# Performance work log

Measured on AMD Instinct MI355X. Metric: run time of the kernel, lower is better.

The kernel has to match this reference:

```python
import jax, jax.numpy as jnp
import numpy as np

NODE_CARDS = [119, 5, 12, 12, 10, 6, 6, 2, 2]
EDGE_CARDS = [5, 6, 2]
HIDDEN = 256
LAYERS = 5
N = 60000
E = 180000
G = 2048  # num graphs (fixed num_segments)
BN_EPS = 1e-5

_NODE_OFFS = np.concatenate([[0], np.cumsum(NODE_CARDS[:-1])]).astype(np.int32)
_EDGE_OFFS = np.concatenate([[0], np.cumsum(EDGE_CARDS[:-1])]).astype(np.int32)
_NODE_MAX = np.asarray(NODE_CARDS, np.int32) - 1
_EDGE_MAX = np.asarray(EDGE_CARDS, np.int32) - 1


def _cat_sum(x, table, maxs, offs):
    # x: [N, F] int; table: [sum(cards), H] -> [N, H]
    idx = jnp.clip(x, 0, maxs[None, :]) + offs[None, :]
    return table[idx].sum(axis=1)


def setup_inputs() -> dict:
    key = jax.random.key(0)
    ks = jax.random.split(key, 32)
    w = 0.0625  # ~ xavier for 256

    def nrm(k, shape, s=w):
        return jax.random.normal(k, shape, dtype=jnp.float32) * s

    inp = {
        'x': jax.random.randint(ks[0], (N, len(NODE_CARDS)), 0, 119, dtype=jnp.int32),
        'edge_index': jax.random.randint(ks[1], (2, E), 0, N, dtype=jnp.int32),
        'edge_attr': jax.random.randint(ks[2], (E, len(EDGE_CARDS)), 0, 6, dtype=jnp.int32),
        'batch': jnp.sort(jax.random.randint(ks[3], (N,), 0, G, dtype=jnp.int32)),
        # embeddings
        'node_emb': nrm(ks[4], (int(sum(NODE_CARDS)), HIDDEN), 0.1),
        'edge_emb': nrm(ks[5], (int(sum(EDGE_CARDS)), HIDDEN), 0.1),
        'vn_emb': nrm(ks[6], (1, HIDDEN), 0.1),
        # GINE conv: eps + 2-layer MLP per layer (stacked)
        'eps': jnp.zeros((LAYERS,), jnp.float32),
        'W1': nrm(ks[7], (LAYERS, HIDDEN, HIDDEN)),
        'b1': jnp.zeros((LAYERS, HIDDEN), jnp.float32),
        'W2': nrm(ks[8], (LAYERS, HIDDEN, HIDDEN)),
        'b2': jnp.zeros((LAYERS, HIDDEN), jnp.float32),
        # BatchNorm (eval mode: running stats)
        'bn_gamma': jnp.ones((LAYERS, HIDDEN), jnp.float32),
        'bn_beta': jnp.zeros((LAYERS, HIDDEN), jnp.float32),
        'bn_mean': nrm(ks[9], (LAYERS, HIDDEN), 0.02),
        'bn_var': jnp.ones((LAYERS, HIDDEN), jnp.float32),
        # virtual-node MLP per layer
        'vW1': nrm(ks[10], (LAYERS, HIDDEN, HIDDEN)),
        'vb1': jnp.zeros((LAYERS, HIDDEN), jnp.float32),
        'vW2': nrm(ks[11], (LAYERS, HIDDEN, HIDDEN)),
        'vb2': jnp.zeros((LAYERS, HIDDEN), jnp.float32),
        # head MLP (2 layers: hidden->hidden->1)
        'hW1': nrm(ks[12], (HIDDEN, HIDDEN)),
        'hb1': jnp.zeros((HIDDEN,), jnp.float32),
        'hW2': nrm(ks[13], (HIDDEN, 1)),
        'hb2': jnp.zeros((1,), jnp.float32),
    }
    return inp


def reference(x, edge_index, edge_attr, batch,
              node_emb, edge_emb, vn_emb, eps,
              W1, b1, W2, b2,
              bn_gamma, bn_beta, bn_mean, bn_var,
              vW1, vb1, vW2, vb2,
              hW1, hb1, hW2, hb2):
    node_maxs = jnp.asarray(_NODE_MAX)
    node_offs = jnp.asarray(_NODE_OFFS)
    edge_maxs = jnp.asarray(_EDGE_MAX)
    edge_offs = jnp.asarray(_EDGE_OFFS)

    h = _cat_sum(x, node_emb, node_maxs, node_offs)          # [N, H]
    ea = _cat_sum(edge_attr, edge_emb, edge_maxs, edge_offs)  # [E, H]
    src, dst = edge_index[0], edge_index[1]

    vn = jnp.broadcast_to(vn_emb[0], (G, HIDDEN))  # [G, H]

    def mean_pool(h_):
        s = jax.ops.segment_sum(h_, batch, num_segments=G)
        cnt = jax.ops.segment_sum(jnp.ones((h_.shape[0], 1), h_.dtype), batch, num_segments=G)
        return s / jnp.maximum(cnt, 1.0)

    for l in range(LAYERS):
        h = h + vn[batch]
        # GINEConv: msg = relu(x_src + edge_attr); agg scatter-add onto dst
        msg = jax.nn.relu(h[src] + ea)                        # [E, H]
        agg = jax.ops.segment_sum(msg, dst, num_segments=N)   # [N, H]
        z = (1.0 + eps[l]) * h + agg
        z = jax.nn.relu(z @ W1[l] + b1[l]) @ W2[l] + b2[l]
        # BatchNorm1d (eval, running stats)
        z = (z - bn_mean[l]) * (bn_gamma[l] / jnp.sqrt(bn_var[l] + BN_EPS)) + bn_beta[l]
        h = jax.nn.relu(z)
        # virtual-node update
        g = mean_pool(h)
        vn = vn + (jax.nn.relu(g @ vW1[l] + vb1[l]) @ vW2[l] + vb2[l])

    g = mean_pool(h)                                          # [G, H]
    logits = (jax.nn.relu(g @ hW1 + hb1) @ hW2 + hb2).reshape(-1)  # [G]
    return logits
```

## Files before the change

kernel.cpp:

```cpp
#include <hip/hip_runtime.h>

#define NN 60000
#define NE 180000
#define NG 2048
#define NL 5
#define CAP 32

typedef unsigned short u16;
typedef unsigned int u32;
typedef __bf16 bf16x8 __attribute__((ext_vector_type(8)));
typedef float f32x4 __attribute__((ext_vector_type(4)));

__device__ __forceinline__ u16 f2bf(float f) {
    u32 u = __builtin_bit_cast(u32, f);
    u += 0x7FFFu + ((u >> 16) & 1u);
    return (u16)(u >> 16);
}
__device__ __forceinline__ float bf2f(u16 s) {
    return __builtin_bit_cast(float, (u32)s << 16);
}
__device__ __forceinline__ void gload_lds16(const void* g, void* l) {
    __builtin_amdgcn_global_load_lds(
        (const __attribute__((address_space(1))) unsigned int*)g,
        (__attribute__((address_space(3))) unsigned int*)l, 16, 0, 0);
}
__device__ __forceinline__ int swz(int row, int col) {
    return (row << 9) + ((((col >> 3) ^ (row & 7))) << 4) + ((col & 7) << 1);
}

__constant__ int NODE_OFF[9]  = {0, 119, 124, 136, 148, 158, 164, 170, 172};
__constant__ int NODE_MAXC[9] = {118, 4, 11, 11, 9, 5, 5, 1, 1};

__global__ __launch_bounds__(256) void k_prep_weights(
    const float* __restrict__ W1, const float* __restrict__ W2,
    const float* __restrict__ vW1, const float* __restrict__ vW2,
    const float* __restrict__ hW1, u16* __restrict__ Wt)
{
    int mat = blockIdx.x >> 8;
    int n = blockIdx.x & 255;
    int k = threadIdx.x;
    const float* src;
    if (mat < 5)       src = W1 + (size_t)mat * 65536;
    else if (mat < 10) src = W2 + (size_t)(mat - 5) * 65536;
    else if (mat < 15) src = vW1 + (size_t)(mat - 10) * 65536;
    else if (mat < 20) src = vW2 + (size_t)(mat - 15) * 65536;
    else               src = hW1;
    Wt[(size_t)mat * 65536 + n * 256 + k] = f2bf(src[k * 256 + n]);
}

__global__ __launch_bounds__(256) void k_misc(
    const float* __restrict__ eemb, const int* __restrict__ batch,
    const float* __restrict__ vn_emb,
    u16* __restrict__ comb, int* __restrict__ starts,
    float* __restrict__ vn, u16* __restrict__ vnbf, float* __restrict__ gsum)
{
    int b = blockIdx.x;
    if (b < 2048) {
        int i = b * 256 + threadIdx.x;
        float v = vn_emb[i & 255];
        vn[i] = v;
        vnbf[i] = f2bf(v);
        gsum[i] = 0.f;
    } else if (b < 2108) {
        int r = b - 2048, c = threadIdx.x;
        int a0 = r / 12, a1 = (r % 12) / 2, a2 = r & 1;
        comb[r * 256 + c] = f2bf(eemb[a0 * 256 + c] + eemb[(5 + a1) * 256 + c] +
                                 eemb[(11 + a2) * 256 + c]);
    } else {
        int g = (b - 2108) * 256 + threadIdx.x;
        if (g > NG) return;
        int lo = 0, hi = NN;
        while (lo < hi) {
            int mid = (lo + hi) >> 1;
            if (batch[mid] < g) lo = mid + 1; else hi = mid;
        }
        starts[g] = lo;
    }
}

__global__ __launch_bounds__(256) void k_embed(const int* __restrict__ x,
                                               const float* __restrict__ node_emb,
                                               u16* __restrict__ hbf,
                                               int* __restrict__ deg)
{
    int i = blockIdx.x * 4 + (threadIdx.x >> 6);
    if (i >= NN) return;
    if ((threadIdx.x & 63) == 0) deg[i] = 0;
    int c = (threadIdx.x & 63) * 4;
    float4 s = make_float4(0.f, 0.f, 0.f, 0.f);
#pragma unroll
    for (int f = 0; f < 9; ++f) {
        int xv = x[i * 9 + f];
        xv = xv < 0 ? 0 : (xv > NODE_MAXC[f] ? NODE_MAXC[f] : xv);
        const float4 t = *(const float4*)&node_emb[(size_t)(NODE_OFF[f] + xv) * 256 + c];
        s.x += t.x; s.y += t.y; s.z += t.z; s.w += t.w;
    }
    ushort4 o;
    o.x = f2bf(s.x); o.y = f2bf(s.y); o.z = f2bf(s.z); o.w = f2bf(s.w);
    *(ushort4*)&hbf[(size_t)i * 256 + c] = o;
}

__global__ __launch_bounds__(256) void k_bucket(
    const int* __restrict__ src, const int* __restrict__ dst,
    const int* __restrict__ eattr, int* __restrict__ deg, u32* __restrict__ slots)
{
    int e = blockIdx.x * 256 + threadIdx.x;
    if (e >= NE) return;
    int a0 = eattr[e * 3 + 0]; a0 = a0 < 0 ? 0 : (a0 > 4 ? 4 : a0);
    int a1 = eattr[e * 3 + 1]; a1 = a1 < 0 ? 0 : (a1 > 5 ? 5 : a1);
    int a2 = eattr[e * 3 + 2]; a2 = a2 < 0 ? 0 : (a2 > 1 ? 1 : a2);
    u32 code = (u32)(a0 * 12 + a1 * 2 + a2);
    int d = dst[e];
    int p = atomicAdd(&deg[d], 1);
    if (p < CAP) slots[(size_t)d * CAP + p] = (u32)src[e] | (code << 17);
}

__global__ __launch_bounds__(256) void k_agg(
    const u16* __restrict__ hbf, const u16* __restrict__ vnbf,
    const int* __restrict__ batch, const u32* __restrict__ slots,
    const int* __restrict__ deg, const u16* __restrict__ comb,
    u16* __restrict__ Abf, const float* __restrict__ epsp)
{
    int d = blockIdx.x * 4 + (threadIdx.x >> 6);
    int lane = threadIdx.x & 63;
    int c = lane * 4;
    int nd = deg[d];
    nd = nd > CAP ? CAP : nd;

    const u32* sl = slots + (size_t)d * CAP;
    u32 sv_l = (lane < nd) ? sl[lane] : 0u;
    int b_l = (lane < nd) ? batch[sv_l & 0x1FFFFu] : 0;

    float4 acc = make_float4(0.f, 0.f, 0.f, 0.f);
    for (int p = 0; p < nd; ++p) {
        u32 sv = (u32)__shfl((int)sv_l, p);
        int b  = __shfl(b_l, p);
        int s  = (int)(sv & 0x1FFFFu);
        int code = (int)(sv >> 17);
        const ushort4 hv = *(const ushort4*)&hbf[(size_t)s * 256 + c];
        const ushort4 vv = *(const ushort4*)&vnbf[(size_t)b * 256 + c];
        const ushort4 tv = *(const ushort4*)&comb[(size_t)code * 256 + c];
        acc.x += fmaxf(bf2f(hv.x) + bf2f(vv.x) + bf2f(tv.x), 0.f);
        acc.y += fmaxf(bf2f(hv.y) + bf2f(vv.y) + bf2f(tv.y), 0.f);
        acc.z += fmaxf(bf2f(hv.z) + bf2f(vv.z) + bf2f(tv.z), 0.f);
        acc.w += fmaxf(bf2f(hv.w) + bf2f(vv.w) + bf2f(tv.w), 0.f);
    }

    int bd = batch[d];
    float ep = 1.0f + *epsp;
    const ushort4 hd = *(const ushort4*)&hbf[(size_t)d * 256 + c];
    const ushort4 vd = *(const ushort4*)&vnbf[(size_t)bd * 256 + c];
    ushort4 o;
    o.x = f2bf((bf2f(hd.x) + bf2f(vd.x)) * ep + acc.x);
    o.y = f2bf((bf2f(hd.y) + bf2f(vd.y)) * ep + acc.y);
    o.z = f2bf((bf2f(hd.z) + bf2f(vd.z)) * ep + acc.z);
    o.w = f2bf((bf2f(hd.w) + bf2f(vd.w)) * ep + acc.w);
    *(ushort4*)&Abf[(size_t)d * 256 + c] = o;
}

__device__ __forceinline__ void stageW(const u16* __restrict__ W, u16* Bl,
                                       int k0, int tid, int wid)
{
#pragma unroll
    for (int i = 0; i < 4; ++i) {
        int slot = i * 512 + tid;
        int row = slot >> 3, cch = slot & 7;
        int g = cch ^ (row & 7);
        gload_lds16((const char*)W + (size_t)row * 512 + (size_t)k0 * 2 + (g << 4),
                    (char*)Bl + ((i * 512 + wid * 64) << 4));
    }
}

__device__ __forceinline__ void gemm64(const u16* Tl, u16* Bl, const u16* __restrict__ W,
                                       f32x4 (&acc)[2][4], int wm, int wn,
                                       int lane, int tid, int wid)
{
    const int cl = lane & 15;
    for (int k0 = 0; k0 < 256; k0 += 64) {
        __syncthreads();
        stageW(W, Bl, k0, tid, wid);
        __syncthreads();
#pragma unroll
        for (int kw = 0; kw < 2; ++kw) {
            int q = kw * 4 + (lane >> 4);
            int qt = (k0 >> 3) + q;
            bf16x8 af[2], bfr[4];
#pragma unroll
            for (int t = 0; t < 2; ++t) {
                int ar = wm + t * 16 + cl;
                af[t] = __builtin_bit_cast(bf16x8,
                    *(const uint4*)((const char*)Tl + (ar << 9) + ((qt ^ (ar & 7)) << 4)));
            }
#pragma unroll
            for (int t = 0; t < 4; ++t) {
                int br = wn + t * 16 + cl;
                bfr[t] = __builtin_bit_cast(bf16x8,
                    *(const uint4*)((const char*)Bl + (br << 7) + ((q ^ (br & 7)) << 4)));
            }
#pragma unroll
            for (int i = 0; i < 2; ++i)
#pragma unroll
                for (int j = 0; j < 4; ++j)
                    acc[i][j] = __builtin_amdgcn_mfma_f32_16x16x32_bf16(af[i], bfr[j], acc[i][j], 0, 0, 0);
        }
    }
}

__device__ __forceinline__ void writeT(u16* Tl, const f32x4 (&acc)[2][4],
                                       const float* __restrict__ b1,
                                       int wm, int wn, int lane)
{
    const int cl = lane & 15, rg = lane >> 4;
#pragma unroll
    for (int j = 0; j < 4; ++j) {
        int col = wn + j * 16 + cl;
        float bv = b1[col];
#pragma unroll
        for (int i = 0; i < 2; ++i)
#pragma unroll
            for (int r = 0; r < 4; ++r) {
                int row = wm + i * 16 + rg * 4 + r;
                float v = fmaxf(acc[i][j][r] + bv, 0.f);
                *(u16*)((char*)Tl + swz(row, col)) = f2bf(v);
            }
    }
}

__global__ __launch_bounds__(512) void k_mlpP(
    const u16* __restrict__ Abf, u16* __restrict__ hnxt,
    const int* __restrict__ batch,
    const u16* __restrict__ W1t, const u16* __restrict__ W2t,
    const float* __restrict__ b1, const float* __restrict__ b2,
    const float* __restrict__ bng, const float* __restrict__ bnb,
    const float* __restrict__ bnm, const float* __restrict__ bnv,
    float* __restrict__ gsum)
{
    __shared__ __align__(16) u16 Bl[256 * 64];
    __shared__ __align__(16) u16 Tl[64 * 256];
    __shared__ int batchLds[64];
    const int m0 = blockIdx.x * 64;
    const int tid = threadIdx.x, lane = tid & 63, wid = tid >> 6;
    const int wm = (wid >> 2) * 32, wn = (wid & 3) * 64;
    const int cl = lane & 15, rg = lane >> 4;

    if (tid < 64) batchLds[tid] = (m0 + tid < NN) ? batch[m0 + tid] : -1;

#pragma unroll
    for (int i = 0; i < 4; ++i) {
        int slot = i * 512 + tid;
        int row = slot >> 5, cch = slot & 31;
        int g = cch ^ (row & 7);
        gload_lds16((const char*)Abf + (size_t)(m0 + row) * 512 + (g << 4),
                    (char*)Tl + ((i * 512 + wid * 64) << 4));
    }

    f32x4 acc1[2][4] = {};
    gemm64(Tl, Bl, W1t, acc1, wm, wn, lane, tid, wid);
    __syncthreads();
    writeT(Tl, acc1, b1, wm, wn, lane);

    f32x4 acc2[2][4] = {};
    gemm64(Tl, Bl, W2t, acc2, wm, wn, lane, tid, wid);
    __syncthreads();

#pragma unroll
    for (int j = 0; j < 4; ++j) {
        int gn = wn + j * 16 + cl;
        float bv = b2[gn];
        float sc = bng[gn] * rsqrtf(bnv[gn] + 1e-5f);
        float sh = bnb[gn] - bnm[gn] * sc;
#pragma unroll
        for (int i = 0; i < 2; ++i) {
#pragma unroll
            for (int r = 0; r < 4; ++r) {
                int lr = wm + i * 16 + rg * 4 + r;
                int gm = m0 + lr;
                if (gm >= NN) continue;
                float v = acc2[i][j][r] + bv;
                u16 hb = f2bf(fmaxf(v * sc + sh, 0.f));
                hnxt[(size_t)gm * 256 + gn] = hb;
                *(u16*)((char*)Tl + swz(lr, gn)) = hb;
            }
        }
    }
    __syncthreads();

    {
        int col = tid & 255, half = tid >> 8;
        float s = 0.f;
        int gcur = -1;
        int r0 = half * 32;
        for (int r = r0; r < r0 + 32; ++r) {
            int g = batchLds[r];
            if (g < 0) break;
            if (g != gcur) {
                if (gcur >= 0) atomicAdd(&gsum[(size_t)gcur * 256 + col], s);
                gcur = g; s = 0.f;
            }
            s += bf2f(*(const u16*)((const char*)Tl + swz(r, col)));
        }
        if (gcur >= 0) atomicAdd(&gsum[(size_t)gcur * 256 + col], s);
    }
}

__global__ __launch_bounds__(512) void k_vnmlp(
    float* __restrict__ gsum, const int* __restrict__ starts,
    const u16* __restrict__ W1t, const u16* __restrict__ W2t,
    const float* __restrict__ b1, const float* __restrict__ b2,
    float* __restrict__ vn, u16* __restrict__ vnbf)
{
    __shared__ __align__(16) u16 Bl[256 * 64];
    __shared__ __align__(16) u16 Tl[64 * 256];
    const int m0 = blockIdx.x * 64;
    const int tid = threadIdx.x, lane = tid & 63, wid = tid >> 6;
    const int wm = (wid >> 2) * 32, wn = (wid & 3) * 64;
    const int cl = lane & 15, rg = lane >> 4;

    {
        const int c = lane * 4;
#pragma unroll
        for (int n = 0; n < 8; ++n) {
            int row = wid * 8 + n;
            int g = m0 + row;
            float4 sv = *(const float4*)&gsum[(size_t)g * 256 + c];
            *(float4*)&gsum[(size_t)g * 256 + c] = make_float4(0.f, 0.f, 0.f, 0.f);
            float cnt = (float)(starts[g + 1] - starts[g]);
            float inv = 1.0f / fmaxf(cnt, 1.0f);
            ushort4 o;
            o.x = f2bf(sv.x * inv); o.y = f2bf(sv.y * inv);
            o.z = f2bf(sv.z * inv); o.w = f2bf(sv.w * inv);
            *(ushort4*)((char*)Tl + swz(row, c)) = o;
        }
    }
    __syncthreads();

    f32x4 acc1[2][4] = {};
    gemm64(Tl, Bl, W1t, acc1, wm, wn, lane, tid, wid);
    __syncthreads();
    writeT(Tl, acc1, b1, wm, wn, lane);

    f32x4 acc2[2][4] = {};
    gemm64(Tl, Bl, W2t, acc2, wm, wn, lane, tid, wid);

#pragma unroll
    for (int j = 0; j < 4; ++j) {
        int gn = wn + j * 16 + cl;
        float bv = b2[gn];
#pragma unroll
        for (int i = 0; i < 2; ++i) {
#pragma unroll
            for (int r = 0; r < 4; ++r) {
                int gm = m0 + wm + i * 16 + rg * 4 + r;
                size_t idx = (size_t)gm * 256 + gn;
                float nv = vn[idx] + acc2[i][j][r] + bv;
                vn[idx] = nv;
                vnbf[idx] = f2bf(nv);
            }
        }
    }
}

__global__ __launch_bounds__(512) void k_headf(
    const float* __restrict__ gsum, const int* __restrict__ starts,
    const u16* __restrict__ W1t, const float* __restrict__ b1,
    const float* __restrict__ hW2, const float* __restrict__ hb2,
    float* __restrict__ out)
{
    __shared__ __align__(16) u16 Bl[256 * 64];
    __shared__ __align__(16) u16 Tl[64 * 256];
    const int m0 = blockIdx.x * 64;
    const int tid = threadIdx.x, lane = tid & 63, wid = tid >> 6;
    const int wm = (wid >> 2) * 32, wn = (wid & 3) * 64;

    {
        const int c = lane * 4;
#pragma unroll
        for (int n = 0; n < 8; ++n) {
            int row = wid * 8 + n;
            int g = m0 + row;
            float4 sv = *(const float4*)&gsum[(size_t)g * 256 + c];
            float cnt = (float)(starts[g + 1] - starts[g]);
            float inv = 1.0f / fmaxf(cnt, 1.0f);
            ushort4 o;
            o.x = f2bf(sv.x * inv); o.y = f2bf(sv.y * inv);
            o.z = f2bf(sv.z * inv); o.w = f2bf(sv.w * inv);
            *(ushort4*)((char*)Tl + swz(row, c)) = o;
        }
    }
    __syncthreads();

    f32x4 acc1[2][4] = {};
    gemm64(Tl, Bl, W1t, acc1, wm, wn, lane, tid, wid);
    __syncthreads();
    writeT(Tl, acc1, b1, wm, wn, lane);
    __syncthreads();

    int row = tid >> 3, oct = tid & 7;
    float s = 0.f;
#pragma unroll
    for (int c = 0; c < 32; ++c) {
        int col = oct * 32 + c;
        s += bf2f(*(const u16*)((const char*)Tl + swz(row, col))) * hW2[col];
    }
    s += __shfl_down(s, 4);
    s += __shfl_down(s, 2);
    s += __shfl_down(s, 1);
    if (oct == 0) out[m0 + row] = s + hb2[0];
}

extern "C" void kernel_launch(void* const* d_in, const int* in_sizes, int n_in,
                              void* d_out, int out_size, void* d_ws, size_t ws_size,
                              hipStream_t stream)
{
    const int*   x        = (const int*)d_in[0];
    const int*   ei       = (const int*)d_in[1];
    const int*   eattr    = (const int*)d_in[2];
    const int*   batch    = (const int*)d_in[3];
    const float* node_emb = (const float*)d_in[4];
    const float* edge_emb = (const float*)d_in[5];
    const float* vn_emb   = (const float*)d_in[6];
    const float* eps      = (const float*)d_in[7];
    const float* W1       = (const float*)d_in[8];
    const float* b1       = (const float*)d_in[9];
    const float* W2       = (const float*)d_in[10];
    const float* b2       = (const float*)d_in[11];
    const float* bng      = (const float*)d_in[12];
    const float* bnb      = (const float*)d_in[13];
    const float* bnm      = (const float*)d_in[14];
    const float* bnv      = (const float*)d_in[15];
    const float* vW1      = (const float*)d_in[16];
    const float* vb1      = (const float*)d_in[17];
    const float* vW2      = (const float*)d_in[18];
    const float* vb2      = (const float*)d_in[19];
    const float* hW1      = (const float*)d_in[20];
    const float* hb1      = (const float*)d_in[21];
    const float* hW2      = (const float*)d_in[22];
    const float* hb2      = (const float*)d_in[23];
    float* out = (float*)d_out;

    char* ws = (char*)d_ws;
    size_t off = 0;
    auto alloc = [&](size_t b) {
        char* p = ws + off;
        off = (off + b + 255) & ~(size_t)255;
        return p;
    };
    u16*   hbf0 = (u16*)alloc((size_t)NN * 256 * 2);
    u16*   hbf1 = (u16*)alloc((size_t)NN * 256 * 2);
    u16*   Abf  = (u16*)alloc((size_t)NN * 256 * 2);
    float* vn   = (float*)alloc((size_t)NG * 256 * 4);
    u16*   vnbf = (u16*)alloc((size_t)NG * 256 * 2);
    float* gsum = (float*)alloc((size_t)NG * 256 * 4);
    u16*   Wt   = (u16*)alloc((size_t)21 * 65536 * 2);
    int*   starts = (int*)alloc((size_t)(NG + 1) * 4);
    u16*   comb = (u16*)alloc((size_t)60 * 256 * 2);
    int*   deg  = (int*)alloc((size_t)NN * 4);
    u32*   slots = (u32*)alloc((size_t)NN * CAP * 4);

    const int* srcI = ei;
    const int* dstI = ei + NE;

    k_prep_weights<<<21 * 256, 256, 0, stream>>>(W1, W2, vW1, vW2, hW1, Wt);
    k_misc<<<2117, 256, 0, stream>>>(edge_emb, batch, vn_emb, comb, starts, vn, vnbf, gsum);
    k_embed<<<NN / 4, 256, 0, stream>>>(x, node_emb, hbf0, deg);
    k_bucket<<<(NE + 255) / 256, 256, 0, stream>>>(srcI, dstI, eattr, deg, slots);

    const int GBIG = (NN + 63) / 64;
    const int GSM  = NG / 64;

    u16* hcur = hbf0;
    u16* hnxt = hbf1;
    for (int l = 0; l < NL; ++l) {
        k_agg<<<NN / 4, 256, 0, stream>>>(hcur, vnbf, batch, slots, deg, comb, Abf, eps + l);
        k_mlpP<<<GBIG, 512, 0, stream>>>(Abf, hnxt, batch,
                                         Wt + (size_t)(0 + l) * 65536,
                                         Wt + (size_t)(5 + l) * 65536,
                                         b1 + l * 256, b2 + l * 256,
                                         bng + l * 256, bnb + l * 256,
                                         bnm + l * 256, bnv + l * 256,
                                         gsum);
        if (l < NL - 1) {
            k_vnmlp<<<GSM, 512, 0, stream>>>(gsum, starts,
                                             Wt + (size_t)(10 + l) * 65536,
                                             Wt + (size_t)(15 + l) * 65536,
                                             vb1 + l * 256, vb2 + l * 256,
                                             vn, vnbf);
        }
        u16* t = hcur; hcur = hnxt; hnxt = t;
    }
    k_headf<<<GSM, 512, 0, stream>>>(gsum, starts, Wt + (size_t)20 * 65536,
                                     hb1, hW2, hb2, out);
}
```

Baseline: 549.2 us.

## Hold MLP weights in registers with 128-row tiles; widen aggregation to 8 bf16 per lane

The fused MLP kernel now processes 128 rows per block. Each wave keeps its 32-column slices of both weight matrices in registers instead of staging weight tiles through LDS every k-step, and the mean-pool partial sums are taken straight from accumulators. This removes repeated weight staging and its barriers, at the cost of heavy register pressure and fewer blocks. The aggregation kernel also handles two nodes per wave with 16-byte loads per lane, which halves the number of load instructions per edge.

```diff
diff --git a/kernel.cpp b/kernel.cpp
--- a/kernel.cpp
+++ b/kernel.cpp
@@ -18,6 +18,15 @@
 }
 __device__ __forceinline__ float bf2f(u16 s) {
     return __builtin_bit_cast(float, (u32)s << 16);
+}
+__device__ __forceinline__ float bflo(u32 w) {
+    return __builtin_bit_cast(float, w << 16);
+}
+__device__ __forceinline__ float bfhi(u32 w) {
+    return __builtin_bit_cast(float, w & 0xFFFF0000u);
+}
+__device__ __forceinline__ u32 pack2bf(float lo, float hi) {
+    return (u32)f2bf(lo) | ((u32)f2bf(hi) << 16);
 }
 __device__ __forceinline__ void gload_lds16(const void* g, void* l) {
     __builtin_amdgcn_global_load_lds(
@@ -121,112 +130,55 @@
     const int* __restrict__ deg, const u16* __restrict__ comb,
     u16* __restrict__ Abf, const float* __restrict__ epsp)
 {
-    int d = blockIdx.x * 4 + (threadIdx.x >> 6);
-    int lane = threadIdx.x & 63;
-    int c = lane * 4;
+    const int wid = threadIdx.x >> 6, lane = threadIdx.x & 63;
+    const int half = lane >> 5, l32 = lane & 31;
+    const int d = blockIdx.x * 8 + wid * 2 + half;
+    const int c = l32 * 8;
     int nd = deg[d];
     nd = nd > CAP ? CAP : nd;
 
     const u32* sl = slots + (size_t)d * CAP;
-    u32 sv_l = (lane < nd) ? sl[lane] : 0u;
-    int b_l = (lane < nd) ? batch[sv_l & 0x1FFFFu] : 0;
-
-    float4 acc = make_float4(0.f, 0.f, 0.f, 0.f);
+    u32 sv_l = (l32 < nd) ? sl[l32] : 0u;
+    int b_l = (l32 < nd) ? batch[sv_l & 0x1FFFFu] : 0;
+
+    float acc[8] = {0.f, 0.f, 0.f, 0.f, 0.f, 0.f, 0.f, 0.f};
     for (int p = 0; p < nd; ++p) {
-        u32 sv = (u32)__shfl((int)sv_l, p);
-        int b  = __shfl(b_l, p);
+        int srcl = (lane & 32) | p;
+        u32 sv = (u32)__shfl((int)sv_l, srcl);
+        int b  = __shfl(b_l, srcl);
         int s  = (int)(sv & 0x1FFFFu);
         int code = (int)(sv >> 17);
-        const ushort4 hv = *(const ushort4*)&hbf[(size_t)s * 256 + c];
-        const ushort4 vv = *(const ushort4*)&vnbf[(size_t)b * 256 + c];
-        const ushort4 tv = *(const ushort4*)&comb[(size_t)code * 256 + c];
-        acc.x += fmaxf(bf2f(hv.x) + bf2f(vv.x) + bf2f(tv.x), 0.f);
-        acc.y += fmaxf(bf2f(hv.y) + bf2f(vv.y) + bf2f(tv.y), 0.f);
-        acc.z += fmaxf(bf2f(hv.z) + bf2f(vv.z) + bf2f(tv.z), 0.f);
-        acc.w += fmaxf(bf2f(hv.w) + bf2f(vv.w) + bf2f(tv.w), 0.f);
+        const uint4 hv = *(const uint4*)&hbf[(size_t)s * 256 + c];
+        const uint4 vv = *(const uint4*)&vnbf[(size_t)b * 256 + c];
+        const uint4 tv = *(const uint4*)&comb[(size_t)code * 256 + c];
+        const u32* hw = (const u32*)&hv;
+        const u32* vw = (const u32*)&vv;
+        const u32* tw = (const u32*)&tv;
+#pragma unroll
+        for (int e = 0; e < 4; ++e) {
+            acc[e * 2 + 0] += fmaxf(bflo(hw[e]) + bflo(vw[e]) + bflo(tw[e]), 0.f);
+            acc[e * 2 + 1] += fmaxf(bfhi(hw[e]) + bfhi(vw[e]) + bfhi(tw[e]), 0.f);
+        }
     }
 
     int bd = batch[d];
     float ep = 1.0f + *epsp;
-    const ushort4 hd = *(const ushort4*)&hbf[(size_t)d * 256 + c];
-    const ushort4 vd = *(const ushort4*)&vnbf[(size_t)bd * 256 + c];
-    ushort4 o;
-    o.x = f2bf((bf2f(hd.x) + bf2f(vd.x)) * ep + acc.x);
-    o.y = f2bf((bf2f(hd.y) + bf2f(vd.y)) * ep + acc.y);
-    o.z = f2bf((bf2f(hd.z) + bf2f(vd.z)) * ep + acc.z);
-    o.w = f2bf((bf2f(hd.w) + bf2f(vd.w)) * ep + acc.w);
-    *(ushort4*)&Abf[(size_t)d * 256 + c] = o;
-}
-
-__device__ __forceinline__ void stageW(const u16* __restrict__ W, u16* Bl,
-                                       int k0, int tid, int wid)
-{
-#pragma unroll
-    for (int i = 0; i < 4; ++i) {
-        int slot = i * 512 + tid;
-        int row = slot >> 3, cch = slot & 7;
-        int g = cch ^ (row & 7);
-        gload_lds16((const char*)W + (size_t)row * 512 + (size_t)k0 * 2 + (g << 4),
-                    (char*)Bl + ((i * 512 + wid * 64) << 4));
-    }
-}
-
-__device__ __forceinline__ void gemm64(const u16* Tl, u16* Bl, const u16* __restrict__ W,
-                                       f32x4 (&acc)[2][4], int wm, int wn,
-                                       int lane, int tid, int wid)
-{
-    const int cl = lane & 15;
-    for (int k0 = 0; k0 < 256; k0 += 64) {
-        __syncthreads();
-        stageW(W, Bl, k0, tid, wid);
-        __syncthreads();
-#pragma unroll
-        for (int kw = 0; kw < 2; ++kw) {
-            int q = kw * 4 + (lane >> 4);
-            int qt = (k0 >> 3) + q;
-            bf16x8 af[2], bfr[4];
-#pragma unroll
-            for (int t = 0; t < 2; ++t) {
-                int ar = wm + t * 16 + cl;
-                af[t] = __builtin_bit_cast(bf16x8,
-                    *(const uint4*)((const char*)Tl + (ar << 9) + ((qt ^ (ar & 7)) << 4)));
-            }
-#pragma unroll
-            for (int t = 0; t < 4; ++t) {
-                int br = wn + t * 16 + cl;
-                bfr[t] = __builtin_bit_cast(bf16x8,
-                    *(const uint4*)((const char*)Bl + (br << 7) + ((q ^ (br & 7)) << 4)));
-            }
-#pragma unroll
-            for (int i = 0; i < 2; ++i)
-#pragma unroll
-                for (int j = 0; j < 4; ++j)
-                    acc[i][j] = __builtin_amdgcn_mfma_f32_16x16x32_bf16(af[i], bfr[j], acc[i][j], 0, 0, 0);
-        }
-    }
-}
-
-__device__ __forceinline__ void writeT(u16* Tl, const f32x4 (&acc)[2][4],
-                                       const float* __restrict__ b1,
-                                       int wm, int wn, int lane)
-{
-    const int cl = lane & 15, rg = lane >> 4;
-#pragma unroll
-    for (int j = 0; j < 4; ++j) {
-        int col = wn + j * 16 + cl;
-        float bv = b1[col];
-#pragma unroll
-        for (int i = 0; i < 2; ++i)
-#pragma unroll
-            for (int r = 0; r < 4; ++r) {
-                int row = wm + i * 16 + rg * 4 + r;
-                float v = fmaxf(acc[i][j][r] + bv, 0.f);
-                *(u16*)((char*)Tl + swz(row, col)) = f2bf(v);
-            }
-    }
-}
-
-__global__ __launch_bounds__(512) void k_mlpP(
+    const uint4 hd = *(const uint4*)&hbf[(size_t)d * 256 + c];
+    const uint4 vd = *(const uint4*)&vnbf[(size_t)bd * 256 + c];
+    const u32* hw = (const u32*)&hd;
+    const u32* vw = (const u32*)&vd;
+    uint4 o;
+    u32* op = (u32*)&o;
+#pragma unroll
+    for (int e = 0; e < 4; ++e) {
+        float lo = (bflo(hw[e]) + bflo(vw[e])) * ep + acc[e * 2 + 0];
+        float hi = (bfhi(hw[e]) + bfhi(vw[e])) * ep + acc[e * 2 + 1];
+        op[e] = pack2bf(lo, hi);
+    }
+    *(uint4*)&Abf[(size_t)d * 256 + c] = o;
+}
+
+__global__ __launch_bounds__(512, 2) void k_mlp2(
     const u16* __restrict__ Abf, u16* __restrict__ hnxt,
     const int* __restrict__ batch,
     const u16* __restrict__ W1t, const u16* __restrict__ W2t,
@@ -235,71 +187,180 @@
     const float* __restrict__ bnm, const float* __restrict__ bnv,
     float* __restrict__ gsum)
 {
-    __shared__ __align__(16) u16 Bl[256 * 64];
-    __shared__ __align__(16) u16 Tl[64 * 256];
-    __shared__ int batchLds[64];
-    const int m0 = blockIdx.x * 64;
+    __shared__ __align__(16) u16 Tl[128 * 256];
+    __shared__ int batchLds[128];
+    const int m0 = blockIdx.x * 128;
     const int tid = threadIdx.x, lane = tid & 63, wid = tid >> 6;
-    const int wm = (wid >> 2) * 32, wn = (wid & 3) * 64;
+    const int wn = wid * 32;
     const int cl = lane & 15, rg = lane >> 4;
 
-    if (tid < 64) batchLds[tid] = (m0 + tid < NN) ? batch[m0 + tid] : -1;
-
-#pragma unroll
-    for (int i = 0; i < 4; ++i) {
+    if (tid < 128) batchLds[tid] = (m0 + tid < NN) ? batch[m0 + tid] : -1;
+
+    bf16x8 B1[2][8], B2[2][8];
+#pragma unroll
+    for (int j = 0; j < 2; ++j) {
+        const char* w1p = (const char*)W1t + (size_t)(wn + j * 16 + cl) * 512 + (rg << 4);
+        const char* w2p = (const char*)W2t + (size_t)(wn + j * 16 + cl) * 512 + (rg << 4);
+#pragma unroll
+        for (int ks = 0; ks < 8; ++ks) {
+            B1[j][ks] = __builtin_bit_cast(bf16x8, *(const uint4*)(w1p + ks * 64));
+            B2[j][ks] = __builtin_bit_cast(bf16x8, *(const uint4*)(w2p + ks * 64));
+        }
+    }
+
+#pragma unroll
+    for (int i = 0; i < 8; ++i) {
         int slot = i * 512 + tid;
         int row = slot >> 5, cch = slot & 31;
         int g = cch ^ (row & 7);
         gload_lds16((const char*)Abf + (size_t)(m0 + row) * 512 + (g << 4),
                     (char*)Tl + ((i * 512 + wid * 64) << 4));
     }
-
-    f32x4 acc1[2][4] = {};
-    gemm64(Tl, Bl, W1t, acc1, wm, wn, lane, tid, wid);
-    __syncthreads();
-    writeT(Tl, acc1, b1, wm, wn, lane);
-
-    f32x4 acc2[2][4] = {};
-    gemm64(Tl, Bl, W2t, acc2, wm, wn, lane, tid, wid);
-    __syncthreads();
-
-#pragma unroll
-    for (int j = 0; j < 4; ++j) {
+    __syncthreads();
+
+    f32x4 acc[8][2] = {};
+#pragma unroll
+    for (int ks = 0; ks < 8; ++ks) {
+#pragma unroll
+        for (int i = 0; i < 8; ++i) {
+            int ar = i * 16 + cl;
+            int ch = ks * 4 + rg;
+            bf16x8 af = __builtin_bit_cast(bf16x8,
+                *(const uint4*)((const char*)Tl + (ar << 9) + ((ch ^ (ar & 7)) << 4)));
+#pragma unroll
+            for (int j = 0; j < 2; ++j)
+                acc[i][j] = __builtin_amdgcn_mfma_f32_16x16x32_bf16(af, B1[j][ks], acc[i][j], 0, 0, 0);
+        }
+    }
+    __syncthreads();
+
+#pragma unroll
+    for (int j = 0; j < 2; ++j) {
+        int col = wn + j * 16 + cl;
+        float bv = b1[col];
+#pragma unroll
+        for (int i = 0; i < 8; ++i)
+#pragma unroll
+            for (int r = 0; r < 4; ++r) {
+                int row = i * 16 + rg * 4 + r;
+                float v = fmaxf(acc[i][j][r] + bv, 0.f);
+                *(u16*)((char*)Tl + swz(row, col)) = f2bf(v);
+            }
+    }
+    __syncthreads();
+
+#pragma unroll
+    for (int i = 0; i < 8; ++i)
+#pragma unroll
+        for (int j = 0; j < 2; ++j)
+            acc[i][j] = f32x4{0.f, 0.f, 0.f, 0.f};
+#pragma unroll
+    for (int ks = 0; ks < 8; ++ks) {
+#pragma unroll
+        for (int i = 0; i < 8; ++i) {
+            int ar = i * 16 + cl;
+            int ch = ks * 4 + rg;
+            bf16x8 af = __builtin_bit_cast(bf16x8,
+                *(const uint4*)((const char*)Tl + (ar << 9) + ((ch ^ (ar & 7)) << 4)));
+#pragma unroll
+            for (int j = 0; j < 2; ++j)
+                acc[i][j] = __builtin_amdgcn_mfma_f32_16x16x32_bf16(af, B2[j][ks], acc[i][j], 0, 0, 0);
+        }
+    }
+
+#pragma unroll
+    for (int j = 0; j < 2; ++j) {
         int gn = wn + j * 16 + cl;
         float bv = b2[gn];
         float sc = bng[gn] * rsqrtf(bnv[gn] + 1e-5f);
         float sh = bnb[gn] - bnm[gn] * sc;
-#pragma unroll
-        for (int i = 0; i < 2; ++i) {
-#pragma unroll
-            for (int r = 0; r < 4; ++r) {
-                int lr = wm + i * 16 + rg * 4 + r;
-                int gm = m0 + lr;
-                if (gm >= NN) continue;
-                float v = acc2[i][j][r] + bv;
-                u16 hb = f2bf(fmaxf(v * sc + sh, 0.f));
-                hnxt[(size_t)gm * 256 + gn] = hb;
-                *(u16*)((char*)Tl + swz(lr, gn)) = hb;
-            }
-        }
-    }
-    __syncthreads();
-
-    {
-        int col = tid & 255, half = tid >> 8;
         float s = 0.f;
         int gcur = -1;
-        int r0 = half * 32;
-        for (int r = r0; r < r0 + 32; ++r) {
-            int g = batchLds[r];
-            if (g < 0) break;
-            if (g != gcur) {
-                if (gcur >= 0) atomicAdd(&gsum[(size_t)gcur * 256 + col], s);
-                gcur = g; s = 0.f;
+#pragma unroll
+        for (int i = 0; i < 8; ++i) {
+#pragma unroll
+            for (int r = 0; r < 4; ++r) {
+                int row = i * 16 + rg * 4 + r;
+                int g = batchLds[row];
+                float v = acc[i][j][r] + bv;
+                u16 hb = f2bf(fmaxf(v * sc + sh, 0.f));
+                if (g >= 0) hnxt[(size_t)(m0 + row) * 256 + gn] = hb;
+                if (g != gcur) {
+                    if (gcur >= 0) atomicAdd(&gsum[(size_t)gcur * 256 + gn], s);
+                    gcur = g; s = 0.f;
+                }
+                if (g >= 0) s += bf2f(hb);
             }
-            s += bf2f(*(const u16*)((const char*)Tl + swz(r, col)));
-        }
-        if (gcur >= 0) atomicAdd(&gsum[(size_t)gcur * 256 + col], s);
+        }
+        if (gcur >= 0) atomicAdd(&gsum[(size_t)gcur * 256 + gn], s);
+    }
+}
+
+__device__ __forceinline__ void stageW(const u16* __restrict__ W, u16* Bl,
+                                       int k0, int tid, int wid)
+{
+#pragma unroll
+    for (int i = 0; i < 4; ++i) {
+        int slot = i * 512 + tid;
+        int row = slot >> 3, cch = slot & 7;
+        int g = cch ^ (row & 7);
+        gload_lds16((const char*)W + (size_t)row * 512 + (size_t)k0 * 2 + (g << 4),
+                    (char*)Bl + ((i * 512 + wid * 64) << 4));
+    }
+}
+
+__device__ __forceinline__ void gemm64(const u16* Tl, u16* Bl, const u16* __restrict__ W,
+                                       f32x4 (&acc)[2][4], int wm, int wn,
+                                       int lane, int tid, int wid)
+{
+    const int cl = lane & 15;
+    for (int k0 = 0; k0 < 256; k0 += 64) {
+        __syncthreads();
+        stageW(W, Bl, k0, tid, wid);
+        __syncthreads();
+#pragma unroll
+        for (int kw = 0; kw < 2; ++kw) {
+            int q = kw * 4 + (lane >> 4);
+            int qt = (k0 >> 3) + q;
+            bf16x8 af[2], bfr[4];
+#pragma unroll
+            for (int t = 0; t < 2; ++t) {
+                int ar = wm + t * 16 + cl;
+                af[t] = __builtin_bit_cast(bf16x8,
+                    *(const uint4*)((const char*)Tl + (ar << 9) + ((qt ^ (ar & 7)) << 4)));
+            }
+#pragma unroll
+            for (int t = 0; t < 4; ++t) {
+                int br = wn + t * 16 + cl;
+                bfr[t] = __builtin_bit_cast(bf16x8,
+                    *(const uint4*)((const char*)Bl + (br << 7) + ((q ^ (br & 7)) << 4)));
+            }
+#pragma unroll
+            for (int i = 0; i < 2; ++i)
+#pragma unroll
+                for (int j = 0; j < 4; ++j)
+                    acc[i][j] = __builtin_amdgcn_mfma_f32_16x16x32_bf16(af[i], bfr[j], acc[i][j], 0, 0, 0);
+        }
+    }
+}
+
+__device__ __forceinline__ void writeT(u16* Tl, const f32x4 (&acc)[2][4],
+                                       const float* __restrict__ b1,
+                                       int wm, int wn, int lane)
+{
+    const int cl = lane & 15, rg = lane >> 4;
+#pragma unroll
+    for (int j = 0; j < 4; ++j) {
+        int col = wn + j * 16 + cl;
+        float bv = b1[col];
+#pragma unroll
+        for (int i = 0; i < 2; ++i)
+#pragma unroll
+            for (int r = 0; r < 4; ++r) {
+                int row = wm + i * 16 + rg * 4 + r;
+                float v = fmaxf(acc[i][j][r] + bv, 0.f);
+                *(u16*)((char*)Tl + swz(row, col)) = f2bf(v);
+            }
     }
 }
 
@@ -447,7 +508,7 @@
     };
     u16*   hbf0 = (u16*)alloc((size_t)NN * 256 * 2);
     u16*   hbf1 = (u16*)alloc((size_t)NN * 256 * 2);
-    u16*   Abf  = (u16*)alloc((size_t)NN * 256 * 2);
+    u16*   Abf  = (u16*)alloc((size_t)NN * 256 * 2 + 65536);
     float* vn   = (float*)alloc((size_t)NG * 256 * 4);
     u16*   vnbf = (u16*)alloc((size_t)NG * 256 * 2);
     float* gsum = (float*)alloc((size_t)NG * 256 * 4);
@@ -465,14 +526,14 @@
     k_embed<<<NN / 4, 256, 0, stream>>>(x, node_emb, hbf0, deg);
     k_bucket<<<(NE + 255) / 256, 256, 0, stream>>>(srcI, dstI, eattr, deg, slots);
 
-    const int GBIG = (NN + 63) / 64;
+    const int GBIG = (NN + 127) / 128;
     const int GSM  = NG / 64;
 
     u16* hcur = hbf0;
     u16* hnxt = hbf1;
     for (int l = 0; l < NL; ++l) {
-        k_agg<<<NN / 4, 256, 0, stream>>>(hcur, vnbf, batch, slots, deg, comb, Abf, eps + l);
-        k_mlpP<<<GBIG, 512, 0, stream>>>(Abf, hnxt, batch,
+        k_agg<<<NN / 8, 256, 0, stream>>>(hcur, vnbf, batch, slots, deg, comb, Abf, eps + l);
+        k_mlp2<<<GBIG, 512, 0, stream>>>(Abf, hnxt, batch,
                                          Wt + (size_t)(0 + l) * 65536,
                                          Wt + (size_t)(5 + l) * 65536,
                                          b1 + l * 256, b2 + l * 256,
```

New measurement: 551.8 us. No clear change (+0.5%).
